# Kernel optimization log

Hardware: AMD Instinct MI355X
Metric: run time of the kernel (lower is better)

## Reference

```python
import jax, jax.numpy as jnp
import numpy as np

HEADS = 8
HEAD_DIM = 32
SCALE = HEAD_DIM ** (-0.5)


def setup_inputs() -> dict:
    key = jax.random.key(0)
    k1, k2, k3 = jax.random.split(key, 3)
    B, DIM, N = 4, 512, 2048
    INNER = HEADS * HEAD_DIM  # 256
    x = jax.random.normal(k1, (B, DIM, N), dtype=jnp.float32)
    # Conv1d(kernel=1, bias=False) == channel-mixing matmul; weight (out_ch, in_ch)
    w_qkv = jax.random.normal(k2, (3 * INNER, DIM), dtype=jnp.float32) * (DIM ** -0.5)
    w_out = jax.random.normal(k3, (DIM, INNER), dtype=jnp.float32) * (INNER ** -0.5)
    b_out = jnp.zeros((DIM,), dtype=jnp.float32)
    return {"x": x, "w_qkv": w_qkv, "w_out": w_out, "b_out": b_out}


def reference(x, w_qkv, w_out, b_out):
    B, DIM, N = x.shape
    INNER = HEADS * HEAD_DIM
    # to_qkv: 1x1 conv over channels, then permute(0,2,1) -> (B, N, 3*INNER)
    qkv = jnp.einsum('bcn,oc->bno', x, w_qkv)
    q, k, v = jnp.split(qkv, 3, axis=-1)
    # 'b n (h d) -> b h n d'
    def to_heads(t):
        return t.reshape(B, N, HEADS, HEAD_DIM).transpose(0, 2, 1, 3)
    q, k, v = to_heads(q), to_heads(k), to_heads(v)
    # L2 similarity: -||q_i - k_j||_2 * scale, via expansion (avoids O(N^2 d) tensor)
    q2 = jnp.sum(q * q, axis=-1)            # (B,H,N)
    k2 = jnp.sum(k * k, axis=-1)            # (B,H,N)
    qk = jnp.einsum('bhid,bhjd->bhij', q, k)  # (B,H,N,N)
    dist2 = q2[..., :, None] + k2[..., None, :] - 2.0 * qk
    smi = -jnp.sqrt(jnp.maximum(dist2, 1e-12)) * SCALE
    attn = jax.nn.softmax(smi, axis=-1)
    out = jnp.einsum('bhij,bhjd->bhid', attn, v)  # (B,H,N,d)
    # 'b h n d -> b (h d) n'
    out = out.transpose(0, 1, 3, 2).reshape(B, INNER, N)
    # to_out: 1x1 conv with bias
    return jnp.einsum('bcn,oc->bon', out, w_out) + b_out[None, :, None]
```

## Files before the change

### kernel.cpp

```cpp
#include <hip/hip_runtime.h>
#include <math.h>

#define N_SEQ 2048
#define DIMC 512
#define INNER 256
#define C2F (0.17677669529663687f * 1.4426950408889634f)

typedef short bf16x8 __attribute__((ext_vector_type(8)));
typedef float f32x4 __attribute__((ext_vector_type(4)));


static __device__ __forceinline__ ushort f2bf(float f) {
    uint x = __float_as_uint(f);
    x += 0x7fff + ((x >> 16) & 1);
    return (ushort)(x >> 16);
}
static __device__ __forceinline__ float bf2f(ushort u) {
    return __uint_as_float(((uint)u) << 16);
}
static __device__ __forceinline__ float fast_exp2(float x) {
    float r; asm("v_exp_f32 %0, %1" : "=v"(r) : "v"(x)); return r;
}
static __device__ __forceinline__ float fast_sqrt(float x) {
    float r; asm("v_sqrt_f32 %0, %1" : "=v"(r) : "v"(x)); return r;
}

__global__ void xpose_cvt(const float* __restrict__ x, ushort* __restrict__ xt) {
    __shared__ __align__(16) ushort T[64][72];
    const int b = blockIdx.z;
    const int c0 = blockIdx.y * 64;
    const int n0 = blockIdx.x * 64;
    const int t = threadIdx.x;
    const int cl = t >> 4;
    const int n4 = (t & 15) * 4;
    const float* xb = x + ((size_t)b * DIMC + c0) * N_SEQ + n0;
#pragma unroll
    for (int cc = 0; cc < 4; ++cc) {
        const int c = cl + cc * 16;
        float4 v = *(const float4*)(xb + (size_t)c * N_SEQ + n4);
        T[n4 + 0][c] = f2bf(v.x);
        T[n4 + 1][c] = f2bf(v.y);
        T[n4 + 2][c] = f2bf(v.z);
        T[n4 + 3][c] = f2bf(v.w);
    }
    __syncthreads();
    const int nl = t >> 2;
    const int c16 = (t & 3) * 16;
    uint4 v0 = *(const uint4*)&T[nl][c16];
    uint4 v1 = *(const uint4*)&T[nl][c16 + 8];
    ushort* dst = xt + ((size_t)b * N_SEQ + n0 + nl) * DIMC + c0 + c16;
    *(uint4*)dst = v0;
    *(uint4*)(dst + 8) = v1;
}

__global__ void wcvt(const float* __restrict__ w, ushort* __restrict__ w16) {
    int i = (blockIdx.x * 256 + threadIdx.x) * 4;
    float4 v = *(const float4*)(w + i);
    ushort4 p;
    p.x = f2bf(v.x); p.y = f2bf(v.y); p.z = f2bf(v.z); p.w = f2bf(v.w);
    *(ushort4*)(w16 + i) = p;
}

__global__ __launch_bounds__(256) void qkv_mfma(const ushort* __restrict__ xt,
        const ushort* __restrict__ w16, ushort* __restrict__ ws16) {
    __shared__ __align__(16) ushort Wls[4 * 520];
    __shared__ __align__(16) ushort Xls[4 * 520];
    const int b = blockIdx.z;
    const int o0 = blockIdx.y * 64;
    const int n0 = blockIdx.x * 64;
    const int t = threadIdx.x;
    const int l = t & 63, w = t >> 6;
    const int q15 = l & 15, g = l >> 4;
    f32x4 acc[4];
#pragma unroll
    for (int nn = 0; nn < 4; ++nn) acc[nn] = (f32x4){0.f, 0.f, 0.f, 0.f};
    const int srow = t >> 2, sg = t & 3;
    const ushort* wsrc = w16 + (size_t)(o0 + srow) * DIMC + sg * 8;
    const ushort* xsrc = xt + ((size_t)b * N_SEQ + n0 + srow) * DIMC + sg * 8;
    uint4 wreg = *(const uint4*)wsrc;
    uint4 xreg = *(const uint4*)xsrc;
    for (int k0 = 0; k0 < DIMC; k0 += 32) {
        __builtin_amdgcn_s_barrier();
        __builtin_amdgcn_sched_barrier(0);
        *(uint4*)(Wls + sg * 520 + srow * 8) = wreg;
        *(uint4*)(Xls + sg * 520 + srow * 8) = xreg;
        if (k0 + 32 < DIMC) {
            wreg = *(const uint4*)(wsrc + k0 + 32);
            xreg = *(const uint4*)(xsrc + k0 + 32);
        }
        asm volatile("s_waitcnt lgkmcnt(0)" ::: "memory");
        __builtin_amdgcn_s_barrier();
        __builtin_amdgcn_sched_barrier(0);
        bf16x8 af = *(const bf16x8*)(Wls + g * 520 + (16 * w + q15) * 8);
        __builtin_amdgcn_s_setprio(1);
#pragma unroll
        for (int nn = 0; nn < 4; ++nn) {
            bf16x8 bfr = *(const bf16x8*)(Xls + g * 520 + (16 * nn + q15) * 8);
            acc[nn] = __builtin_amdgcn_mfma_f32_16x16x32_bf16(af, bfr, acc[nn], 0, 0, 0);
        }
        __builtin_amdgcn_s_setprio(0);
    }
    const int oatom = o0 + 16 * w;
    const int t_idx = oatom >> 8;
    const int h = (oatom >> 5) & 7;
    const int bh = b * 8 + h;
    const int d0 = (oatom & 31) + 4 * g;
    if (t_idx < 2) {
        ushort* dst = ws16 + (size_t)t_idx * 2097152 + (size_t)bh * 65536
                      + (size_t)(d0 >> 3) * 16384 + (d0 & 7);
#pragma unroll
        for (int nn = 0; nn < 4; ++nn) {
            const int n_ = n0 + 16 * nn + q15;
            ushort4 p;
            p.x = f2bf(acc[nn][0]); p.y = f2bf(acc[nn][1]);
            p.z = f2bf(acc[nn][2]); p.w = f2bf(acc[nn][3]);
            *(ushort4*)(dst + (size_t)n_ * 8) = p;
        }
    } else {
        ushort* dst = ws16 + (size_t)4194304 + (size_t)bh * 65536;
#pragma unroll
        for (int nn = 0; nn < 4; ++nn) {
            const int n_ = n0 + 16 * nn + q15;
            ushort* dd = dst + (size_t)(n_ >> 3) * 256 + (n_ & 7);
            dd[(d0 + 0) * 8] = f2bf(acc[nn][0]);
            dd[(d0 + 1) * 8] = f2bf(acc[nn][1]);
            dd[(d0 + 2) * 8] = f2bf(acc[nn][2]);
            dd[(d0 + 3) * 8] = f2bf(acc[nn][3]);
        }
    }
}

__global__ void sq_kernel(const ushort* __restrict__ ws16, float* __restrict__ q2,
                          float* __restrict__ k2) {
    const int which = blockIdx.y;
    const int idx = blockIdx.x * 256 + threadIdx.x;
    const int bh = idx >> 11, n = idx & 2047;
    const ushort* base = ws16 + (size_t)which * 2097152 + (size_t)bh * 65536
                         + (size_t)n * 8;
    float s = 0.f;
#pragma unroll
    for (int g = 0; g < 4; ++g) {
        uint4 v = *(const uint4*)(base + (size_t)g * 16384);
        uint a[4] = {v.x, v.y, v.z, v.w};
#pragma unroll
        for (int e = 0; e < 4; ++e) {
            float lo = bf2f((ushort)(a[e] & 0xffff));
            float hi = bf2f((ushort)(a[e] >> 16));
            s += lo * lo + hi * hi;
        }
    }
    (which == 0 ? q2 : k2)[idx] = s;
}

__global__ __launch_bounds__(256) void attn_kernel(
        const ushort* __restrict__ ws16, const float* __restrict__ q2g,
        const float* __restrict__ k2g, ushort* __restrict__ att16) {
    __shared__ __align__(16) ushort Pls[4][16][140];
    const int bid = blockIdx.x;
    const int sw = (bid & 7) * 128 + (bid >> 3);
    const int q0 = (sw & 31) * 64;
    const int bh = sw >> 5;
    const int b = bh >> 3, h = bh & 7;
    const int tid = threadIdx.x;
    const int l = tid & 63;
    const int w = tid >> 6;
    const int q15 = l & 15;
    const int g = l >> 4;
    const int qrow = q0 + 16 * w + q15;

    const ushort* Qbh = ws16 + (size_t)bh * 65536;
    const ushort* Kbh = ws16 + 2097152 + (size_t)bh * 65536;
    const ushort* Vbh = ws16 + 4194304 + (size_t)bh * 65536;
    const float* k2bh = k2g + (size_t)bh * 2048;

    const bf16x8 qf = *(const bf16x8*)(Qbh + (size_t)g * 16384 + (size_t)qrow * 8);
    const float q2v = q2g[(size_t)bh * 2048 + qrow];

    f32x4 accO[2];
    accO[0] = (f32x4){0.f, 0.f, 0.f, 0.f};
    accO[1] = (f32x4){0.f, 0.f, 0.f, 0.f};
    float lsm = 0.f;

    for (int t = 0; t < N_SEQ / 128; ++t) {
        const int j0 = t * 128;
        bf16x8 kf[8], vfr[8];
        float4 kk[8];
#pragma unroll
        for (int k = 0; k < 8; ++k)
            kf[k] = *(const bf16x8*)(Kbh + (size_t)g * 16384
                                     + (size_t)(j0 + 16 * k + q15) * 8);
#pragma unroll
        for (int jc = 0; jc < 4; ++jc)
#pragma unroll
            for (int d = 0; d < 2; ++d)
                vfr[jc * 2 + d] = *(const bf16x8*)(Vbh + (size_t)j0 * 32
                                   + (size_t)(4 * jc + g) * 256
                                   + (size_t)(16 * d + q15) * 8);
#pragma unroll
        for (int k = 0; k < 8; ++k)
            kk[k] = *(const float4*)(k2bh + j0 + 16 * k + 4 * g);

        const f32x4 zz = (f32x4){0.f, 0.f, 0.f, 0.f};
        f32x4 st[8];
        __builtin_amdgcn_s_setprio(1);
#pragma unroll
        for (int k = 0; k < 8; ++k)
            st[k] = __builtin_amdgcn_mfma_f32_16x16x32_bf16(kf[k], qf, zz, 0, 0, 0);
        __builtin_amdgcn_s_setprio(0);

        float lt = 0.f;
#pragma unroll
        for (int k = 0; k < 8; ++k) {
            float ka[4] = {kk[k].x, kk[k].y, kk[k].z, kk[k].w};
            float p[4];
#pragma unroll
            for (int r = 0; r < 4; ++r) {
                float a = q2v + ka[r];
                float d2 = fmaf(-2.f, st[k][r], a);
                p[r] = fast_exp2(-C2F * fast_sqrt(fmaxf(d2, 1e-12f)));
            }
            lt += (p[0] + p[1]) + (p[2] + p[3]);
            uint pk0, pk1;
            asm("v_cvt_pk_bf16_f32 %0, %1, %2" : "=v"(pk0) : "v"(p[0]), "v"(p[1]));
            asm("v_cvt_pk_bf16_f32 %0, %1, %2" : "=v"(pk1) : "v"(p[2]), "v"(p[3]));
            uint2 pv; pv.x = pk0; pv.y = pk1;
            *(uint2*)&Pls[w][q15][16 * k + 4 * g] = pv;
        }
        lsm += lt;

        __builtin_amdgcn_s_setprio(1);
#pragma unroll
        for (int jc = 0; jc < 4; ++jc) {
            bf16x8 pf = *(const bf16x8*)&Pls[w][q15][32 * jc + 8 * g];
#pragma unroll
            for (int d = 0; d < 2; ++d)
                accO[d] = __builtin_amdgcn_mfma_f32_16x16x32_bf16(vfr[jc * 2 + d],
                                                                  pf, accO[d], 0, 0, 0);
        }
        __builtin_amdgcn_s_setprio(0);
    }

    lsm += __shfl_xor(lsm, 16);
    lsm += __shfl_xor(lsm, 32);
    const float invl = 1.f / lsm;
    ushort* dst = att16 + ((size_t)(b * N_SEQ + qrow)) * INNER + h * 32 + 4 * g;
#pragma unroll
    for (int d = 0; d < 2; ++d) {
        ushort4 o;
        o.x = f2bf(accO[d][0] * invl); o.y = f2bf(accO[d][1] * invl);
        o.z = f2bf(accO[d][2] * invl); o.w = f2bf(accO[d][3] * invl);
        *(ushort4*)(dst + d * 16) = o;
    }
}

__global__ __launch_bounds__(256) void out_mfma(const ushort* __restrict__ att16,
        const ushort* __restrict__ wo16, const float* __restrict__ bias,
        float* __restrict__ out) {
    __shared__ __align__(16) ushort Wls[4 * 520];
    __shared__ __align__(16) ushort Als[4 * 520];
    const int b = blockIdx.z;
    const int o0 = blockIdx.y * 64;
    const int n0 = blockIdx.x * 64;
    const int t = threadIdx.x;
    const int l = t & 63, w = t >> 6;
    const int q15 = l & 15, g = l >> 4;
    f32x4 acc[4];
#pragma unroll
    for (int nn = 0; nn < 4; ++nn) acc[nn] = (f32x4){0.f, 0.f, 0.f, 0.f};
    const int srow = t >> 2, sg = t & 3;
    const ushort* wsrc = wo16 + (size_t)(o0 + srow) * INNER + sg * 8;
    const ushort* asrc = att16 + ((size_t)b * N_SEQ + n0 + srow) * INNER + sg * 8;
    uint4 wreg = *(const uint4*)wsrc;
    uint4 areg = *(const uint4*)asrc;
    for (int k0 = 0; k0 < INNER; k0 += 32) {
        __builtin_amdgcn_s_barrier();
        __builtin_amdgcn_sched_barrier(0);
        *(uint4*)(Wls + sg * 520 + srow * 8) = wreg;
        *(uint4*)(Als + sg * 520 + srow * 8) = areg;
        if (k0 + 32 < INNER) {
            wreg = *(const uint4*)(wsrc + k0 + 32);
            areg = *(const uint4*)(asrc + k0 + 32);
        }
        asm volatile("s_waitcnt lgkmcnt(0)" ::: "memory");
        __builtin_amdgcn_s_barrier();
        __builtin_amdgcn_sched_barrier(0);
        bf16x8 af = *(const bf16x8*)(Wls + g * 520 + (16 * w + q15) * 8);
        __builtin_amdgcn_s_setprio(1);
#pragma unroll
        for (int nn = 0; nn < 4; ++nn) {
            bf16x8 bfr = *(const bf16x8*)(Als + g * 520 + (16 * nn + q15) * 8);
            acc[nn] = __builtin_amdgcn_mfma_f32_16x16x32_bf16(af, bfr, acc[nn], 0, 0, 0);
        }
        __builtin_amdgcn_s_setprio(0);
    }
    const int obase = o0 + 16 * w + 4 * g;
    float4 bi = *(const float4*)(bias + obase);
    float* ob = out + ((size_t)b * DIMC + obase) * N_SEQ;
#pragma unroll
    for (int nn = 0; nn < 4; ++nn) {
        const int n_ = n0 + 16 * nn + q15;
        ob[0 * N_SEQ + n_] = acc[nn][0] + bi.x;
        ob[1 * N_SEQ + n_] = acc[nn][1] + bi.y;
        ob[2 * N_SEQ + n_] = acc[nn][2] + bi.z;
        ob[3 * N_SEQ + n_] = acc[nn][3] + bi.w;
    }
}

extern "C" void kernel_launch(void* const* d_in, const int* in_sizes, int n_in,
                              void* d_out, int out_size, void* d_ws, size_t ws_size,
                              hipStream_t stream) {
    const float* x = (const float*)d_in[0];
    const float* w_qkv = (const float*)d_in[1];
    const float* w_out = (const float*)d_in[2];
    const float* b_out = (const float*)d_in[3];
    ushort* ws16 = (ushort*)d_ws;
    float* q2f = (float*)((char*)d_ws + (12 << 20));
    float* k2f = (float*)((char*)d_ws + (12 << 20) + (256 << 10));
    ushort* att16 = (ushort*)((char*)d_ws + (13 << 20));
    ushort* wo16 = (ushort*)((char*)d_ws + (17 << 20));
    ushort* xt16 = (ushort*)((char*)d_ws + (21 << 20));
    ushort* wq16 = (ushort*)((char*)d_ws + (29 << 20));
    float* out = (float*)d_out;

    xpose_cvt<<<dim3(32, 8, 4), 256, 0, stream>>>(x, xt16);
    wcvt<<<dim3(384), 256, 0, stream>>>(w_qkv, wq16);
    wcvt<<<dim3(128), 256, 0, stream>>>(w_out, wo16);
    qkv_mfma<<<dim3(32, 12, 4), 256, 0, stream>>>(xt16, wq16, ws16);
    sq_kernel<<<dim3(256, 2), 256, 0, stream>>>(ws16, q2f, k2f);
    attn_kernel<<<dim3(1024), 256, 0, stream>>>(ws16, q2f, k2f, att16);
    out_mfma<<<dim3(32, 8, 4), 256, 0, stream>>>(att16, wo16, b_out, out);
}
```

Baseline: 98.91 us.

## Split attention over key halves with combine kernel; fold scale into squared norms

The attention kernel now splits the key range into two halves, doubling the grid to 2048 blocks. Each block writes unnormalised fp32 partial outputs and row sums, and a new combine_norm kernel adds the halves, normalises and writes bf16. The softmax scale is folded into q2/k2 and the QK coefficient, so the exponent uses a negated source modifier instead of a multiply. The two weight-conversion launches are merged into one. The split adds fp32 partial traffic and an extra launch in exchange for more parallelism. The combine kernel also contains a stray att16[0] self-assignment, which adds a redundant racy global access.

```diff
diff --git a/kernel.cpp b/kernel.cpp
--- a/kernel.cpp
+++ b/kernel.cpp
@@ -5,6 +5,7 @@
 #define DIMC 512
 #define INNER 256
 #define C2F (0.17677669529663687f * 1.4426950408889634f)
+#define C2F2 (C2F * C2F)
 
 typedef short bf16x8 __attribute__((ext_vector_type(8)));
 typedef float f32x4 __attribute__((ext_vector_type(4)));
@@ -18,8 +19,8 @@
 static __device__ __forceinline__ float bf2f(ushort u) {
     return __uint_as_float(((uint)u) << 16);
 }
-static __device__ __forceinline__ float fast_exp2(float x) {
-    float r; asm("v_exp_f32 %0, %1" : "=v"(r) : "v"(x)); return r;
+static __device__ __forceinline__ float fast_exp2_neg(float x) {
+    float r; asm("v_exp_f32 %0, -%1" : "=v"(r) : "v"(x)); return r;
 }
 static __device__ __forceinline__ float fast_sqrt(float x) {
     float r; asm("v_sqrt_f32 %0, %1" : "=v"(r) : "v"(x)); return r;
@@ -53,12 +54,22 @@
     *(uint4*)(dst + 8) = v1;
 }
 
-__global__ void wcvt(const float* __restrict__ w, ushort* __restrict__ w16) {
-    int i = (blockIdx.x * 256 + threadIdx.x) * 4;
-    float4 v = *(const float4*)(w + i);
-    ushort4 p;
-    p.x = f2bf(v.x); p.y = f2bf(v.y); p.z = f2bf(v.z); p.w = f2bf(v.w);
-    *(ushort4*)(w16 + i) = p;
+__global__ void wcvt2(const float* __restrict__ wq, const float* __restrict__ wo,
+                      ushort* __restrict__ wq16, ushort* __restrict__ wo16) {
+    const int bid = blockIdx.x;
+    if (bid < 384) {
+        int i = (bid * 256 + threadIdx.x) * 4;
+        float4 v = *(const float4*)(wq + i);
+        ushort4 p;
+        p.x = f2bf(v.x); p.y = f2bf(v.y); p.z = f2bf(v.z); p.w = f2bf(v.w);
+        *(ushort4*)(wq16 + i) = p;
+    } else {
+        int i = ((bid - 384) * 256 + threadIdx.x) * 4;
+        float4 v = *(const float4*)(wo + i);
+        ushort4 p;
+        p.x = f2bf(v.x); p.y = f2bf(v.y); p.z = f2bf(v.z); p.w = f2bf(v.w);
+        *(ushort4*)(wo16 + i) = p;
+    }
 }
 
 __global__ __launch_bounds__(256) void qkv_mfma(const ushort* __restrict__ xt,
@@ -149,18 +160,19 @@
             s += lo * lo + hi * hi;
         }
     }
-    (which == 0 ? q2 : k2)[idx] = s;
-}
-
-__global__ __launch_bounds__(256) void attn_kernel(
+    (which == 0 ? q2 : k2)[idx] = s * (float)C2F2;
+}
+
+__global__ __launch_bounds__(256) void attn_partial(
         const ushort* __restrict__ ws16, const float* __restrict__ q2g,
-        const float* __restrict__ k2g, ushort* __restrict__ att16) {
+        const float* __restrict__ k2g, float* __restrict__ Opart,
+        float* __restrict__ lpart) {
     __shared__ __align__(16) ushort Pls[4][16][140];
     const int bid = blockIdx.x;
-    const int sw = (bid & 7) * 128 + (bid >> 3);
-    const int q0 = (sw & 31) * 64;
-    const int bh = sw >> 5;
-    const int b = bh >> 3, h = bh & 7;
+    const int sw = (bid & 7) * 256 + (bid >> 3);
+    const int jh = sw & 1;
+    const int q0 = ((sw >> 1) & 31) * 64;
+    const int bh = sw >> 6;
     const int tid = threadIdx.x;
     const int l = tid & 63;
     const int w = tid >> 6;
@@ -181,8 +193,8 @@
     accO[1] = (f32x4){0.f, 0.f, 0.f, 0.f};
     float lsm = 0.f;
 
-    for (int t = 0; t < N_SEQ / 128; ++t) {
-        const int j0 = t * 128;
+    for (int t = 0; t < 8; ++t) {
+        const int j0 = jh * 1024 + t * 128;
         bf16x8 kf[8], vfr[8];
         float4 kk[8];
 #pragma unroll
@@ -216,8 +228,8 @@
 #pragma unroll
             for (int r = 0; r < 4; ++r) {
                 float a = q2v + ka[r];
-                float d2 = fmaf(-2.f, st[k][r], a);
-                p[r] = fast_exp2(-C2F * fast_sqrt(fmaxf(d2, 1e-12f)));
+                float d2 = fmaf(-2.f * (float)C2F2, st[k][r], a);
+                p[r] = fast_exp2_neg(fast_sqrt(fmaxf(d2, 1e-12f)));
             }
             lt += (p[0] + p[1]) + (p[2] + p[3]);
             uint pk0, pk1;
@@ -242,15 +254,32 @@
 
     lsm += __shfl_xor(lsm, 16);
     lsm += __shfl_xor(lsm, 32);
-    const float invl = 1.f / lsm;
-    ushort* dst = att16 + ((size_t)(b * N_SEQ + qrow)) * INNER + h * 32 + 4 * g;
+    float* orow = Opart + (((size_t)jh * 32 + bh) * 2048 + qrow) * 32 + 4 * g;
 #pragma unroll
     for (int d = 0; d < 2; ++d) {
-        ushort4 o;
-        o.x = f2bf(accO[d][0] * invl); o.y = f2bf(accO[d][1] * invl);
-        o.z = f2bf(accO[d][2] * invl); o.w = f2bf(accO[d][3] * invl);
-        *(ushort4*)(dst + d * 16) = o;
-    }
+        float4 o;
+        o.x = accO[d][0]; o.y = accO[d][1]; o.z = accO[d][2]; o.w = accO[d][3];
+        *(float4*)(orow + 16 * d) = o;
+    }
+    if (g == 0)
+        lpart[(size_t)jh * 65536 + (size_t)bh * 2048 + qrow] = lsm;
+}
+
+__global__ void combine_norm(const float* __restrict__ Opart,
+                             const float* __restrict__ lpart,
+                             ushort* __restrict__ att16) {
+    const int R = blockIdx.x * 32 + (threadIdx.x >> 3);
+    const int d0 = (threadIdx.x & 7) * 4;
+    float4 a = *(const float4*)(Opart + (size_t)R * 32 + d0);
+    float4 b = *(const float4*)(Opart + (size_t)2097152 + (size_t)R * 32 + d0);
+    const float inv = 1.f / (lpart[R] + lpart[R + 65536]);
+    ushort4 o;
+    o.x = f2bf((a.x + b.x) * inv); o.y = f2bf((a.y + b.y) * inv);
+    o.z = f2bf((a.z + b.z) * inv); o.w = f2bf((a.w + b.w) * inv);
+    const int bh = R >> 11, n = R & 2047;
+    att16[0] = att16[0];
+    *(ushort4*)(att16 + (((size_t)(bh >> 3) * N_SEQ + n) * INNER
+                         + (bh & 7) * 32 + d0)) = o;
 }
 
 __global__ __launch_bounds__(256) void out_mfma(const ushort* __restrict__ att16,
@@ -316,17 +345,19 @@
     ushort* ws16 = (ushort*)d_ws;
     float* q2f = (float*)((char*)d_ws + (12 << 20));
     float* k2f = (float*)((char*)d_ws + (12 << 20) + (256 << 10));
-    ushort* att16 = (ushort*)((char*)d_ws + (13 << 20));
-    ushort* wo16 = (ushort*)((char*)d_ws + (17 << 20));
+    float* lpart = (float*)((char*)d_ws + (12 << 20) + (512 << 10));
+    float* Opart = (float*)((char*)d_ws + (13 << 20));
+    ushort* att16 = (ushort*)d_ws;
     ushort* xt16 = (ushort*)((char*)d_ws + (21 << 20));
     ushort* wq16 = (ushort*)((char*)d_ws + (29 << 20));
+    ushort* wo16 = (ushort*)((char*)d_ws + (30 << 20));
     float* out = (float*)d_out;
 
     xpose_cvt<<<dim3(32, 8, 4), 256, 0, stream>>>(x, xt16);
-    wcvt<<<dim3(384), 256, 0, stream>>>(w_qkv, wq16);
-    wcvt<<<dim3(128), 256, 0, stream>>>(w_out, wo16);
+    wcvt2<<<dim3(512), 256, 0, stream>>>(w_qkv, w_out, wq16, wo16);
     qkv_mfma<<<dim3(32, 12, 4), 256, 0, stream>>>(xt16, wq16, ws16);
     sq_kernel<<<dim3(256, 2), 256, 0, stream>>>(ws16, q2f, k2f);
-    attn_kernel<<<dim3(1024), 256, 0, stream>>>(ws16, q2f, k2f, att16);
+    attn_partial<<<dim3(2048), 256, 0, stream>>>(ws16, q2f, k2f, Opart, lpart);
+    combine_norm<<<dim3(2048), 256, 0, stream>>>(Opart, lpart, att16);
     out_mfma<<<dim3(32, 8, 4), 256, 0, stream>>>(att16, wo16, b_out, out);
 }
```

Result: slower. 101.2 us (+2.4%).

## Double-buffer K/V tile loads in attention, prescale norms, merge weight conversions

Applied to the files above, without the earlier changes.

The attention loop now uses two register sets, so the next 128-key tile's K, V and k2 loads are issued before the current tile is computed, overlapping global-memory latency with MFMA and exp work. The softmax scale is folded into the squared norms and the cross-term coefficient, and the negation moves into the v_exp source modifier, which removes per-element multiplies. The two weight-conversion launches are merged into one kernel, and the wo16 buffer is moved to a new workspace offset. Doubling the fragment registers raises VGPR pressure and may lower occupancy.

```diff
diff --git a/kernel.cpp b/kernel.cpp
--- a/kernel.cpp
+++ b/kernel.cpp
@@ -5,6 +5,7 @@
 #define DIMC 512
 #define INNER 256
 #define C2F (0.17677669529663687f * 1.4426950408889634f)
+#define C2F2 (C2F * C2F)
 
 typedef short bf16x8 __attribute__((ext_vector_type(8)));
 typedef float f32x4 __attribute__((ext_vector_type(4)));
@@ -18,8 +19,8 @@
 static __device__ __forceinline__ float bf2f(ushort u) {
     return __uint_as_float(((uint)u) << 16);
 }
-static __device__ __forceinline__ float fast_exp2(float x) {
-    float r; asm("v_exp_f32 %0, %1" : "=v"(r) : "v"(x)); return r;
+static __device__ __forceinline__ float fast_exp2_neg(float x) {
+    float r; asm("v_exp_f32 %0, -%1" : "=v"(r) : "v"(x)); return r;
 }
 static __device__ __forceinline__ float fast_sqrt(float x) {
     float r; asm("v_sqrt_f32 %0, %1" : "=v"(r) : "v"(x)); return r;
@@ -53,12 +54,22 @@
     *(uint4*)(dst + 8) = v1;
 }
 
-__global__ void wcvt(const float* __restrict__ w, ushort* __restrict__ w16) {
-    int i = (blockIdx.x * 256 + threadIdx.x) * 4;
-    float4 v = *(const float4*)(w + i);
-    ushort4 p;
-    p.x = f2bf(v.x); p.y = f2bf(v.y); p.z = f2bf(v.z); p.w = f2bf(v.w);
-    *(ushort4*)(w16 + i) = p;
+__global__ void wcvt2(const float* __restrict__ wq, const float* __restrict__ wo,
+                      ushort* __restrict__ wq16, ushort* __restrict__ wo16) {
+    const int bid = blockIdx.x;
+    if (bid < 384) {
+        int i = (bid * 256 + threadIdx.x) * 4;
+        float4 v = *(const float4*)(wq + i);
+        ushort4 p;
+        p.x = f2bf(v.x); p.y = f2bf(v.y); p.z = f2bf(v.z); p.w = f2bf(v.w);
+        *(ushort4*)(wq16 + i) = p;
+    } else {
+        int i = ((bid - 384) * 256 + threadIdx.x) * 4;
+        float4 v = *(const float4*)(wo + i);
+        ushort4 p;
+        p.x = f2bf(v.x); p.y = f2bf(v.y); p.z = f2bf(v.z); p.w = f2bf(v.w);
+        *(ushort4*)(wo16 + i) = p;
+    }
 }
 
 __global__ __launch_bounds__(256) void qkv_mfma(const ushort* __restrict__ xt,
@@ -149,7 +160,64 @@
             s += lo * lo + hi * hi;
         }
     }
-    (which == 0 ? q2 : k2)[idx] = s;
+    (which == 0 ? q2 : k2)[idx] = s * (float)C2F2;
+}
+
+static __device__ __forceinline__ void load_tile(
+        const ushort* __restrict__ Kfrag, const ushort* __restrict__ Vfrag,
+        const float* __restrict__ k2p, int j0,
+        bf16x8 (&kf)[8], bf16x8 (&vf)[8], float4 (&kk)[8]) {
+#pragma unroll
+    for (int k = 0; k < 8; ++k)
+        kf[k] = *(const bf16x8*)(Kfrag + ((size_t)j0 + 16 * k) * 8);
+#pragma unroll
+    for (int jc = 0; jc < 4; ++jc) {
+        vf[jc * 2 + 0] = *(const bf16x8*)(Vfrag + (size_t)j0 * 32 + jc * 1024);
+        vf[jc * 2 + 1] = *(const bf16x8*)(Vfrag + (size_t)j0 * 32 + jc * 1024 + 128);
+    }
+#pragma unroll
+    for (int k = 0; k < 8; ++k)
+        kk[k] = *(const float4*)(k2p + j0 + 16 * k);
+}
+
+static __device__ __forceinline__ void compute_tile(
+        const bf16x8 (&kf)[8], const bf16x8 (&vf)[8], const float4 (&kk)[8],
+        float q2v, bf16x8 qf, f32x4 (&accO)[2], float& lsm,
+        ushort* __restrict__ plane, int g) {
+    const f32x4 zz = (f32x4){0.f, 0.f, 0.f, 0.f};
+    f32x4 st[8];
+    __builtin_amdgcn_s_setprio(1);
+#pragma unroll
+    for (int k = 0; k < 8; ++k)
+        st[k] = __builtin_amdgcn_mfma_f32_16x16x32_bf16(kf[k], qf, zz, 0, 0, 0);
+    __builtin_amdgcn_s_setprio(0);
+    float lt = 0.f;
+#pragma unroll
+    for (int k = 0; k < 8; ++k) {
+        float ka[4] = {kk[k].x, kk[k].y, kk[k].z, kk[k].w};
+        float p[4];
+#pragma unroll
+        for (int r = 0; r < 4; ++r) {
+            float a = q2v + ka[r];
+            float d2 = fmaf(-2.f * (float)C2F2, st[k][r], a);
+            p[r] = fast_exp2_neg(fast_sqrt(fmaxf(d2, 1e-12f)));
+        }
+        lt += (p[0] + p[1]) + (p[2] + p[3]);
+        uint pk0, pk1;
+        asm("v_cvt_pk_bf16_f32 %0, %1, %2" : "=v"(pk0) : "v"(p[0]), "v"(p[1]));
+        asm("v_cvt_pk_bf16_f32 %0, %1, %2" : "=v"(pk1) : "v"(p[2]), "v"(p[3]));
+        uint2 pv; pv.x = pk0; pv.y = pk1;
+        *(uint2*)(plane + 16 * k + 4 * g) = pv;
+    }
+    lsm += lt;
+    __builtin_amdgcn_s_setprio(1);
+#pragma unroll
+    for (int jc = 0; jc < 4; ++jc) {
+        bf16x8 pf = *(const bf16x8*)(plane + 32 * jc + 8 * g);
+        accO[0] = __builtin_amdgcn_mfma_f32_16x16x32_bf16(vf[jc * 2 + 0], pf, accO[0], 0, 0, 0);
+        accO[1] = __builtin_amdgcn_mfma_f32_16x16x32_bf16(vf[jc * 2 + 1], pf, accO[1], 0, 0, 0);
+    }
+    __builtin_amdgcn_s_setprio(0);
 }
 
 __global__ __launch_bounds__(256) void attn_kernel(
@@ -169,75 +237,32 @@
     const int qrow = q0 + 16 * w + q15;
 
     const ushort* Qbh = ws16 + (size_t)bh * 65536;
-    const ushort* Kbh = ws16 + 2097152 + (size_t)bh * 65536;
-    const ushort* Vbh = ws16 + 4194304 + (size_t)bh * 65536;
-    const float* k2bh = k2g + (size_t)bh * 2048;
+    const ushort* Kfrag = ws16 + 2097152 + (size_t)bh * 65536
+                          + (size_t)g * 16384 + (size_t)q15 * 8;
+    const ushort* Vfrag = ws16 + 4194304 + (size_t)bh * 65536
+                          + (size_t)g * 256 + (size_t)q15 * 8;
+    const float* k2p = k2g + (size_t)bh * 2048 + 4 * g;
 
     const bf16x8 qf = *(const bf16x8*)(Qbh + (size_t)g * 16384 + (size_t)qrow * 8);
     const float q2v = q2g[(size_t)bh * 2048 + qrow];
+    ushort* plane = &Pls[w][q15][0];
 
     f32x4 accO[2];
     accO[0] = (f32x4){0.f, 0.f, 0.f, 0.f};
     accO[1] = (f32x4){0.f, 0.f, 0.f, 0.f};
     float lsm = 0.f;
 
-    for (int t = 0; t < N_SEQ / 128; ++t) {
-        const int j0 = t * 128;
-        bf16x8 kf[8], vfr[8];
-        float4 kk[8];
-#pragma unroll
-        for (int k = 0; k < 8; ++k)
-            kf[k] = *(const bf16x8*)(Kbh + (size_t)g * 16384
-                                     + (size_t)(j0 + 16 * k + q15) * 8);
-#pragma unroll
-        for (int jc = 0; jc < 4; ++jc)
-#pragma unroll
-            for (int d = 0; d < 2; ++d)
-                vfr[jc * 2 + d] = *(const bf16x8*)(Vbh + (size_t)j0 * 32
-                                   + (size_t)(4 * jc + g) * 256
-                                   + (size_t)(16 * d + q15) * 8);
-#pragma unroll
-        for (int k = 0; k < 8; ++k)
-            kk[k] = *(const float4*)(k2bh + j0 + 16 * k + 4 * g);
-
-        const f32x4 zz = (f32x4){0.f, 0.f, 0.f, 0.f};
-        f32x4 st[8];
-        __builtin_amdgcn_s_setprio(1);
-#pragma unroll
-        for (int k = 0; k < 8; ++k)
-            st[k] = __builtin_amdgcn_mfma_f32_16x16x32_bf16(kf[k], qf, zz, 0, 0, 0);
-        __builtin_amdgcn_s_setprio(0);
-
-        float lt = 0.f;
-#pragma unroll
-        for (int k = 0; k < 8; ++k) {
-            float ka[4] = {kk[k].x, kk[k].y, kk[k].z, kk[k].w};
-            float p[4];
-#pragma unroll
-            for (int r = 0; r < 4; ++r) {
-                float a = q2v + ka[r];
-                float d2 = fmaf(-2.f, st[k][r], a);
-                p[r] = fast_exp2(-C2F * fast_sqrt(fmaxf(d2, 1e-12f)));
-            }
-            lt += (p[0] + p[1]) + (p[2] + p[3]);
-            uint pk0, pk1;
-            asm("v_cvt_pk_bf16_f32 %0, %1, %2" : "=v"(pk0) : "v"(p[0]), "v"(p[1]));
-            asm("v_cvt_pk_bf16_f32 %0, %1, %2" : "=v"(pk1) : "v"(p[2]), "v"(p[3]));
-            uint2 pv; pv.x = pk0; pv.y = pk1;
-            *(uint2*)&Pls[w][q15][16 * k + 4 * g] = pv;
-        }
-        lsm += lt;
-
-        __builtin_amdgcn_s_setprio(1);
-#pragma unroll
-        for (int jc = 0; jc < 4; ++jc) {
-            bf16x8 pf = *(const bf16x8*)&Pls[w][q15][32 * jc + 8 * g];
-#pragma unroll
-            for (int d = 0; d < 2; ++d)
-                accO[d] = __builtin_amdgcn_mfma_f32_16x16x32_bf16(vfr[jc * 2 + d],
-                                                                  pf, accO[d], 0, 0, 0);
-        }
-        __builtin_amdgcn_s_setprio(0);
+    bf16x8 kfA[8], vfA[8], kfB[8], vfB[8];
+    float4 kkA[8], kkB[8];
+
+    load_tile(Kfrag, Vfrag, k2p, 0, kfA, vfA, kkA);
+#pragma unroll 1
+    for (int t = 0; t < 16; t += 2) {
+        load_tile(Kfrag, Vfrag, k2p, (t + 1) * 128, kfB, vfB, kkB);
+        compute_tile(kfA, vfA, kkA, q2v, qf, accO, lsm, plane, g);
+        if (t + 2 < 16)
+            load_tile(Kfrag, Vfrag, k2p, (t + 2) * 128, kfA, vfA, kkA);
+        compute_tile(kfB, vfB, kkB, q2v, qf, accO, lsm, plane, g);
     }
 
     lsm += __shfl_xor(lsm, 16);
@@ -317,14 +342,13 @@
     float* q2f = (float*)((char*)d_ws + (12 << 20));
     float* k2f = (float*)((char*)d_ws + (12 << 20) + (256 << 10));
     ushort* att16 = (ushort*)((char*)d_ws + (13 << 20));
-    ushort* wo16 = (ushort*)((char*)d_ws + (17 << 20));
     ushort* xt16 = (ushort*)((char*)d_ws + (21 << 20));
     ushort* wq16 = (ushort*)((char*)d_ws + (29 << 20));
+    ushort* wo16 = (ushort*)((char*)d_ws + (30 << 20));
     float* out = (float*)d_out;
 
     xpose_cvt<<<dim3(32, 8, 4), 256, 0, stream>>>(x, xt16);
-    wcvt<<<dim3(384), 256, 0, stream>>>(w_qkv, wq16);
-    wcvt<<<dim3(128), 256, 0, stream>>>(w_out, wo16);
+    wcvt2<<<dim3(512), 256, 0, stream>>>(w_qkv, w_out, wq16, wo16);
     qkv_mfma<<<dim3(32, 12, 4), 256, 0, stream>>>(xt16, wq16, ws16);
     sq_kernel<<<dim3(256, 2), 256, 0, stream>>>(ws16, q2f, k2f);
     attn_kernel<<<dim3(1024), 256, 0, stream>>>(ws16, q2f, k2f, att16);
```

Result: slower. 119.1 us (+20.4%).
